# Kernel optimization log

Hardware: AMD Instinct MI355X
Metric: run time of the kernel (lower is better)

The kernel has to match this reference:

```python
import jax, jax.numpy as jnp
import numpy as np

D_MODEL = 512
N_HEADS = 8
D_HEAD = D_MODEL // N_HEADS
N_BINS = 32


def setup_inputs() -> dict:
    key = jax.random.key(0)
    ks = jax.random.split(key, 12)
    B, N = 8, 1024
    x = jax.random.normal(ks[0], (B, N, D_MODEL), dtype=jnp.float32)
    positions = jax.random.randint(ks[1], (B, N), 0, 5000, dtype=jnp.int32)
    mask = jnp.ones((B, N), dtype=jnp.float32)
    s = 0.02
    qw = jax.random.normal(ks[2], (D_MODEL, D_MODEL), jnp.float32) * s
    qb = jnp.zeros((D_MODEL,), jnp.float32)
    kw = jax.random.normal(ks[3], (D_MODEL, D_MODEL), jnp.float32) * s
    kb = jnp.zeros((D_MODEL,), jnp.float32)
    vw = jax.random.normal(ks[4], (D_MODEL, D_MODEL), jnp.float32) * s
    vb = jnp.zeros((D_MODEL,), jnp.float32)
    ow = jax.random.normal(ks[5], (D_MODEL, D_MODEL), jnp.float32) * s
    ob = jnp.zeros((D_MODEL,), jnp.float32)
    dist_emb = jax.random.normal(ks[6], (N_BINS, N_HEADS), jnp.float32) * s
    order_bias = jnp.zeros((N_HEADS,), jnp.float32)
    bin_edges = jnp.logspace(0.0, 3.0, N_BINS - 1, dtype=jnp.float32)
    return {"x": x, "positions": positions, "mask": mask,
            "qw": qw, "qb": qb, "kw": kw, "kb": kb, "vw": vw, "vb": vb,
            "ow": ow, "ob": ob, "dist_emb": dist_emb, "order_bias": order_bias,
            "bin_edges": bin_edges}


def reference(x, positions, mask, qw, qb, kw, kb, vw, vb, ow, ob, dist_emb, order_bias, bin_edges):
    B, N, _ = x.shape
    scale = jnp.sqrt(jnp.float32(D_HEAD))
    # projections (torch Linear: y = x @ W^T + b), split heads -> (B,H,N,Dh)
    q = (x @ qw.T + qb).reshape(B, N, N_HEADS, D_HEAD).transpose(0, 2, 1, 3)
    k = (x @ kw.T + kb).reshape(B, N, N_HEADS, D_HEAD).transpose(0, 2, 1, 3)
    v = (x @ vw.T + vb).reshape(B, N, N_HEADS, D_HEAD).transpose(0, 2, 1, 3)
    scores = jnp.einsum('bhqd,bhkd->bhqk', q, k) / scale  # (B,H,N,N)
    pos = positions.astype(jnp.float32)
    pos_i = pos[:, :, None]   # (B,N,1)
    pos_j = pos[:, None, :]   # (B,1,N)
    dist = jnp.abs(pos_j - pos_i)  # (B,N,N)
    # torch.bucketize(right=False) == searchsorted side='left'
    bins = jnp.clip(jnp.searchsorted(bin_edges, dist, side='left'), 0, N_BINS - 1)
    dist_bias = dist_emb[bins]  # (B,N,N,H)
    scores = scores + dist_bias.transpose(0, 3, 1, 2)
    order_sign = (pos_j > pos_i).astype(scores.dtype) - 0.5  # (B,N,N)
    scores = scores + order_sign[:, None, :, :] * order_bias[None, :, None, None]
    mask_2d = mask[:, None, None, :] * mask[:, None, :, None]  # (B,1,N,N)
    scores = jnp.where(mask_2d == 0, jnp.float32(-1e9), scores)
    attn = jax.nn.softmax(scores, axis=-1)
    attn = jnp.nan_to_num(attn, nan=0.0)
    out = jnp.einsum('bhqk,bhkd->bhqd', attn, v)
    out = out.transpose(0, 2, 1, 3).reshape(B, N, D_MODEL)
    out = out * mask[..., None]
    return out @ ow.T + ob
```

## Files before the change

### kernel.cpp

```cpp
#include <hip/hip_runtime.h>
#include <hip/hip_bf16.h>

#define SEQ   1024
#define NH    8
#define DH    64

typedef __attribute__((ext_vector_type(8))) _Float16 half8;
typedef __attribute__((ext_vector_type(4))) _Float16 half4;
typedef __attribute__((ext_vector_type(4))) float    f32x4;

#if __has_builtin(__builtin_amdgcn_exp2f)
#define EXP2F __builtin_amdgcn_exp2f
#else
#define EXP2F exp2f
#endif

__device__ inline unsigned pk2(float a, float b) {
  return __builtin_bit_cast(unsigned, __builtin_amdgcn_cvt_pkrtz(a, b));
}
__device__ inline void swap32(unsigned &a, unsigned &b) {
  asm("v_permlane32_swap_b32 %0, %1" : "+v"(a), "+v"(b));
}
__device__ inline void swap16(unsigned &a, unsigned &b) {
  asm("v_permlane16_swap_b32 %0, %1" : "+v"(a), "+v"(b));
}
__device__ inline half8 mk8(unsigned a, unsigned b, unsigned c, unsigned d) {
  union { unsigned u[4]; half8 h; } x;
  x.u[0] = a; x.u[1] = b; x.u[2] = c; x.u[3] = d;
  return x.h;
}
__device__ __forceinline__ void gload16(const _Float16* g, _Float16* l) {
  __builtin_amdgcn_global_load_lds((const __attribute__((address_space(1))) void*)g,
                                   (__attribute__((address_space(3))) void*)l, 16, 0, 0);
}

__global__ void prep_all(const float* __restrict__ x,
                         const float* __restrict__ qw, const float* __restrict__ kw,
                         const float* __restrict__ vw, const float* __restrict__ ow,
                         const float* __restrict__ qb, const float* __restrict__ kb,
                         const float* __restrict__ vb, const float* __restrict__ edges,
                         _Float16* __restrict__ xh, _Float16* __restrict__ wqkvh,
                         _Float16* __restrict__ owh, float* __restrict__ qkvbias,
                         unsigned char* __restrict__ lutd) {
  const int blk = blockIdx.x, tid = threadIdx.x;
  if (blk < 4096) {
    int g = blk * 256 + tid;
    float4 v = reinterpret_cast<const float4*>(x)[g];
    half4 u;
    u[0] = (_Float16)v.x; u[1] = (_Float16)v.y; u[2] = (_Float16)v.z; u[3] = (_Float16)v.w;
    reinterpret_cast<half4*>(xh)[g] = u;
  } else if (blk < 5122) {
    int g = (blk - 4096) * 256 + tid;
    if (g < 196608) {
      const float* src = (g < 65536) ? qw : (g < 131072) ? kw : vw;
      int lg = g & 65535;
      float4 v = reinterpret_cast<const float4*>(src)[lg];
      half4 u;
      u[0] = (_Float16)v.x; u[1] = (_Float16)v.y; u[2] = (_Float16)v.z; u[3] = (_Float16)v.w;
      reinterpret_cast<half4*>(wqkvh)[g] = u;
    } else if (g < 262144) {
      int lg = g - 196608;
      float4 v = reinterpret_cast<const float4*>(ow)[lg];
      half4 u;
      u[0] = (_Float16)v.x; u[1] = (_Float16)v.y; u[2] = (_Float16)v.z; u[3] = (_Float16)v.w;
      reinterpret_cast<half4*>(owh)[lg] = u;
    } else if (g < 262528) {
      int lg = g - 262144;
      const float* src = (lg < 128) ? qb : (lg < 256) ? kb : vb;
      int ll = lg & 127;
      reinterpret_cast<float4*>(qkvbias)[lg] = reinterpret_cast<const float4*>(src)[ll];
    }
  } else {
    int d = (blk - 5122) * 256 + tid;
    float fd = (float)d;
    int bin = 0;
#pragma unroll
    for (int t = 0; t < 31; ++t) bin += (edges[t] < fd) ? 1 : 0;
    lutd[d] = (unsigned char)bin;
  }
}

__global__ __launch_bounds__(256) void prep_ebins(const int* __restrict__ positions,
                                                  const float* __restrict__ mask,
                                                  const unsigned char* __restrict__ lutd,
                                                  unsigned char* __restrict__ ebins) {
  __shared__ unsigned char lutl[5120];
  __shared__ int posl[SEQ];
  __shared__ unsigned char mk[SEQ];
  const int b = blockIdx.x >> 8, j0 = (blockIdx.x & 255) * 4;
  const int tid = threadIdx.x;
  for (int i = tid; i < 1280; i += 256)
    reinterpret_cast<unsigned*>(lutl)[i] = reinterpret_cast<const unsigned*>(lutd)[i];
  for (int i = tid; i < SEQ; i += 256) {
    posl[i] = positions[b * SEQ + i];
    mk[i] = (mask[b * SEQ + i] == 0.f) ? 32 : 0;
  }
  __syncthreads();
  const int c0 = tid * 4;
#pragma unroll
  for (int jj = 0; jj < 4; ++jj) {
    const int j = j0 + jj;
    const int pr = posl[j];
    unsigned out = 0;
#pragma unroll
    for (int r = 0; r < 4; ++r) {
      int c = c0 + r;
      int pc = posl[c];
      int d = pc - pr; d = d < 0 ? -d : d;
      if (d > 5119) d = 5119;
      unsigned e = lutl[d] | (unsigned)mk[c] | ((pc > pr) ? 64u : 0u);
      out |= e << (8 * r);
    }
    reinterpret_cast<unsigned*>(&ebins[(size_t)(b * SEQ + j) * SEQ])[tid] = out;
  }
}

__global__ __launch_bounds__(256) void qkv_gemm3(const _Float16* __restrict__ xh,
                                                 const _Float16* __restrict__ wh,
                                                 const float* __restrict__ bias,
                                                 _Float16* __restrict__ qkv) {
  __shared__ __attribute__((aligned(16))) _Float16 As[128 * 64];
  __shared__ __attribute__((aligned(16))) _Float16 Bs[128 * 64];
  const int m0 = blockIdx.x * 128, n0 = blockIdx.y * 128;
  const int tid = threadIdx.x, w = tid >> 6, lane = tid & 63;
  const int lr = lane & 15, lg = lane >> 4;
  const int wr = (w >> 1) * 64, wc = (w & 1) * 64;
  f32x4 acc[4][4] = {};
  const int srow8 = lane >> 3;
  const int scol = ((lane & 7) ^ srow8) * 8;
  for (int k0 = 0; k0 < 512; k0 += 64) {
#pragma unroll
    for (int j = 0; j < 4; ++j) {
      const int row = (w * 4 + j) * 8 + srow8;
      gload16(&xh[(size_t)(m0 + row) * 512 + k0 + scol], &As[(w * 4 + j) * 512]);
      gload16(&wh[(size_t)(n0 + row) * 512 + k0 + scol], &Bs[(w * 4 + j) * 512]);
    }
    __syncthreads();
#pragma unroll
    for (int kk = 0; kk < 2; ++kk) {
      half8 af[4], bf[4];
#pragma unroll
      for (int mt = 0; mt < 4; ++mt) {
        const int row = wr + mt * 16 + lr;
        af[mt] = *reinterpret_cast<const half8*>(
            (const char*)As + row * 128 + (((kk * 4 + lg) ^ (row & 7)) * 16));
      }
#pragma unroll
      for (int nt = 0; nt < 4; ++nt) {
        const int row = wc + nt * 16 + lr;
        bf[nt] = *reinterpret_cast<const half8*>(
            (const char*)Bs + row * 128 + (((kk * 4 + lg) ^ (row & 7)) * 16));
      }
#pragma unroll
      for (int mt = 0; mt < 4; ++mt)
#pragma unroll
        for (int nt = 0; nt < 4; ++nt)
          acc[mt][nt] = __builtin_amdgcn_mfma_f32_16x16x32_f16(af[mt], bf[nt], acc[mt][nt], 0, 0, 0);
    }
    __syncthreads();
  }
  const int p = n0 >> 9;
  const float scl = (p == 0) ? 0.125f : (p == 1) ? 1.44269504f : 1.0f;
  if (p < 2) {
#pragma unroll
    for (int nt = 0; nt < 4; ++nt) {
      int n = n0 + wc + nt * 16 + lr;
      float bv = bias[n];
      int c = n & 511, h = c >> 6, d = c & 63;
#pragma unroll
      for (int mt = 0; mt < 4; ++mt)
#pragma unroll
        for (int r = 0; r < 4; ++r) {
          int m = m0 + wr + mt * 16 + lg * 4 + r;
          int bb = m >> 10, nn = m & 1023;
          qkv[p * 4194304 + ((bb * NH + h) * SEQ + nn) * DH + d] = (_Float16)((acc[mt][nt][r] + bv) * scl);
        }
    }
  } else {
#pragma unroll
    for (int nt = 0; nt < 4; ++nt) {
      int n = n0 + wc + nt * 16 + lr;
      float bv = bias[n];
      int c = n & 511, h = c >> 6, d = c & 63;
#pragma unroll
      for (int mt = 0; mt < 4; ++mt) {
        int m = m0 + wr + mt * 16 + lg * 4;
        int bb = m >> 10, nn = m & 1023;
        half4 st;
#pragma unroll
        for (int r = 0; r < 4; ++r) st[r] = (_Float16)(acc[mt][nt][r] + bv);
        *reinterpret_cast<half4*>(&qkv[8388608 + ((bb * NH + h) * DH + d) * SEQ + nn]) = st;
      }
    }
  }
}

#define ASTAGE(bufi, kv0_) do {                                                              \
    _Pragma("unroll") for (int j = 0; j < 2; ++j) {                                          \
      const int row_ = (w * 2 + j) * 8 + (lane >> 3);                                        \
      const int c_ = ((lane & 7) ^ (row_ & 7)) * 8;                                          \
      gload16(Kg + (size_t)((kv0_) + row_) * 64 + c_, &Ks[bufi][(w * 2 + j) * 512]);         \
      gload16(Vtg + (size_t)row_ * 1024 + (kv0_) + c_, &Vt[bufi][(w * 2 + j) * 512]);        \
    }                                                                                        \
  } while (0)

#define EBL(dst, kt_) do {                                                                   \
    _Pragma("unroll") for (int ct = 0; ct < 4; ++ct)                                         \
      dst[ct] = *reinterpret_cast<const unsigned*>(                                          \
          &ebins[(size_t)(b * SEQ + q_base + lr) * SEQ + (kt_) * 64 + ct * 16 + lg * 4]);    \
  } while (0)

#define ACOMP(bufi, ebw) do {                                                                \
    f32x4 s[4];                                                                              \
    _Pragma("unroll") for (int ct = 0; ct < 4; ++ct) {                                       \
      const unsigned eb_ = ebw[ct];                                                          \
      _Pragma("unroll") for (int r = 0; r < 4; ++r) {                                        \
        const unsigned i6_ = (eb_ >> (8 * r)) & 63u;                      \
        float bias_ = elut2[i6_];                                                            \
        if (obh_nz) bias_ += ((eb_ >> (8 * r)) & 64u) ? obh : -obh;                          \
        s[ct][r] = bias_;                                                                    \
      }                                                                                      \
    }                                                                                        \
    __builtin_amdgcn_s_setprio(1);                                                           \
    _Pragma("unroll") for (int ct = 0; ct < 4; ++ct) {                                       \
      const int krow_ = ct * 16 + lr;                                                        \
      half8 kf0 = *reinterpret_cast<const half8*>(                                           \
          (const char*)&Ks[bufi][0] + krow_ * 128 + ((lg ^ (krow_ & 7)) * 16));              \
      half8 kf1 = *reinterpret_cast<const half8*>(                                           \
          (const char*)&Ks[bufi][0] + krow_ * 128 + (((4 + lg) ^ (krow_ & 7)) * 16));        \
      s[ct] = __builtin_amdgcn_mfma_f32_16x16x32_f16(kf0, qf[0], s[ct], 0, 0, 0);            \
      s[ct] = __builtin_amdgcn_mfma_f32_16x16x32_f16(kf1, qf[1], s[ct], 0, 0, 0);            \
    }                                                                                        \
    __builtin_amdgcn_s_setprio(0);                                                           \
                 \
    unsigned W[4][2];                                                                        \
    _Pragma("unroll") for (int ct = 0; ct < 4; ++ct) {                                       \
      float p0 = EXP2F(s[ct][0]), p1 = EXP2F(s[ct][1]);                                      \
      float p2 = EXP2F(s[ct][2]), p3 = EXP2F(s[ct][3]);                                      \
      l_run += (p0 + p1) + (p2 + p3);                                                        \
      W[ct][0] = pk2(p0, p1);                                                                \
      W[ct][1] = pk2(p2, p3);                                                                \
    }                                                                                        \
    swap32(W[0][0], W[1][0]); swap32(W[0][1], W[1][1]);                                      \
    swap32(W[2][0], W[3][0]); swap32(W[2][1], W[3][1]);                                      \
    swap16(W[0][0], W[1][0]); swap16(W[0][1], W[1][1]);                                      \
    swap16(W[2][0], W[3][0]); swap16(W[2][1], W[3][1]);                                      \
    __builtin_amdgcn_s_setprio(1);                                                           \
    _Pragma("unroll") for (int ks = 0; ks < 2; ++ks) {                                       \
      half8 pa = mk8(W[ks * 2][0], W[ks * 2][1], W[ks * 2 + 1][0], W[ks * 2 + 1][1]);        \
      _Pragma("unroll") for (int dt = 0; dt < 4; ++dt) {                                     \
        const int vrow_ = dt * 16 + lr;                                                      \
        half8 vf = *reinterpret_cast<const half8*>(                                          \
            (const char*)&Vt[bufi][0] + vrow_ * 128 + (((ks * 4 + lg) ^ (vrow_ & 7)) * 16)); \
        o[dt] = __builtin_amdgcn_mfma_f32_16x16x32_f16(vf, pa, o[dt], 0, 0, 0);              \
      }                                                                                      \
    }                                                                                        \
    __builtin_amdgcn_s_setprio(0);                                                           \
  } while (0)

__global__ __launch_bounds__(256, 4) void attn8(const _Float16* __restrict__ qkv,
                                                const float* __restrict__ mask,
                                                const unsigned char* __restrict__ ebins,
                                                const float* __restrict__ demb,
                                                const float* __restrict__ obias,
                                                _Float16* __restrict__ aout) {
  __shared__ __attribute__((aligned(16))) _Float16 Ks[2][64 * 64];
  __shared__ __attribute__((aligned(16))) _Float16 Vt[2][64 * 64];
  __shared__ float elut2[64];

  const int blk = blockIdx.x;
  const int lin = (blk & 7) * 128 + (blk >> 3);
  const int qt = lin & 15, h = (lin >> 4) & 7, b = lin >> 7;
  const int tid = threadIdx.x, w = tid >> 6, lane = tid & 63;
  const int lr = lane & 15, lg = lane >> 4;

  if (tid < 64) elut2[tid] = (tid < 32) ? demb[tid * NH + h] * 1.44269504f : -1.442695e9f;
  const float obh = 0.5f * obias[h] * 1.44269504f;
  const bool obh_nz = (obh != 0.f);

  const _Float16* Qg  = qkv + (size_t)(b * NH + h) * 65536;
  const _Float16* Kg  = qkv + 4194304 + (size_t)(b * NH + h) * 65536;
  const _Float16* Vtg = qkv + 8388608 + (size_t)(b * NH + h) * 65536;

  const int q_base = qt * 64 + w * 16;
  half8 qf[2];
#pragma unroll
  for (int ks = 0; ks < 2; ++ks)
    qf[ks] = *reinterpret_cast<const half8*>(&Qg[(q_base + lr) * DH + ks * 32 + lg * 8]);
  const float mq = mask[b * SEQ + q_base + lr];

  float l_run = 0.f;
  f32x4 o[4] = {};

  unsigned ebwA[4], ebwB[4];
  EBL(ebwA, 0);
  ASTAGE(0, 0);
  __syncthreads();

#pragma unroll 1
  for (int i = 0; i < 8; ++i) {
    const int kt = 2 * i;
    EBL(ebwB, kt + 1);
    ASTAGE(1, (kt + 1) * 64);
    ACOMP(0, ebwA);
    __syncthreads();
    if (kt + 2 < 16) {
      EBL(ebwA, kt + 2);
      ASTAGE(0, (kt + 2) * 64);
    }
    ACOMP(1, ebwB);
    __syncthreads();
  }

  float s_ = l_run;
  s_ += __shfl_xor(s_, 16);
  s_ += __shfl_xor(s_, 32);
  const float linv = mq / fmaxf(s_, 1e-35f);
#pragma unroll
  for (int dt = 0; dt < 4; ++dt) {
    half4 st;
#pragma unroll
    for (int r = 0; r < 4; ++r) st[r] = (_Float16)(o[dt][r] * linv);
    *reinterpret_cast<half4*>(
        &aout[(size_t)(b * SEQ + q_base + lr) * 512 + h * DH + dt * 16 + lg * 4]) = st;
  }
}

__global__ __launch_bounds__(256) void out_gemm3(const _Float16* __restrict__ ah,
                                                 const _Float16* __restrict__ wh,
                                                 const float* __restrict__ ob,
                                                 float* __restrict__ out) {
  __shared__ __attribute__((aligned(16))) _Float16 As[128 * 64];
  __shared__ __attribute__((aligned(16))) _Float16 Bs[64 * 64];
  const int m0 = blockIdx.x * 128, n0 = blockIdx.y * 64;
  const int tid = threadIdx.x, w = tid >> 6, lane = tid & 63;
  const int lr = lane & 15, lg = lane >> 4;
  const int wr = (w >> 1) * 64, wc = (w & 1) * 32;
  f32x4 acc[4][2] = {};
  const int srow8 = lane >> 3;
  const int scol = ((lane & 7) ^ srow8) * 8;
  for (int k0 = 0; k0 < 512; k0 += 64) {
#pragma unroll
    for (int j = 0; j < 4; ++j) {
      const int row = (w * 4 + j) * 8 + srow8;
      gload16(&ah[(size_t)(m0 + row) * 512 + k0 + scol], &As[(w * 4 + j) * 512]);
    }
#pragma unroll
    for (int j = 0; j < 2; ++j) {
      const int row = (w * 2 + j) * 8 + srow8;
      gload16(&wh[(size_t)(n0 + row) * 512 + k0 + scol], &Bs[(w * 2 + j) * 512]);
    }
    __syncthreads();
#pragma unroll
    for (int kk = 0; kk < 2; ++kk) {
      half8 af[4], bf[2];
#pragma unroll
      for (int mt = 0; mt < 4; ++mt) {
        const int row = wr + mt * 16 + lr;
        af[mt] = *reinterpret_cast<const half8*>(
            (const char*)As + row * 128 + (((kk * 4 + lg) ^ (row & 7)) * 16));
      }
#pragma unroll
      for (int nt = 0; nt < 2; ++nt) {
        const int row = wc + nt * 16 + lr;
        bf[nt] = *reinterpret_cast<const half8*>(
            (const char*)Bs + row * 128 + (((kk * 4 + lg) ^ (row & 7)) * 16));
      }
#pragma unroll
      for (int mt = 0; mt < 4; ++mt)
#pragma unroll
        for (int nt = 0; nt < 2; ++nt)
          acc[mt][nt] = __builtin_amdgcn_mfma_f32_16x16x32_f16(af[mt], bf[nt], acc[mt][nt], 0, 0, 0);
    }
    __syncthreads();
  }
#pragma unroll
  for (int nt = 0; nt < 2; ++nt) {
    int n = n0 + wc + nt * 16 + lr;
    float bv = ob[n];
#pragma unroll
    for (int mt = 0; mt < 4; ++mt)
#pragma unroll
      for (int r = 0; r < 4; ++r) {
        int m = m0 + wr + mt * 16 + lg * 4 + r;
        out[m * 512 + n] = acc[mt][nt][r] + bv;
      }
  }
}

extern "C" void kernel_launch(void* const* d_in, const int* in_sizes, int n_in,
                              void* d_out, int out_size, void* d_ws, size_t ws_size,
                              hipStream_t stream) {
  const float* x         = (const float*)d_in[0];
  const int*   positions = (const int*)d_in[1];
  const float* mask      = (const float*)d_in[2];
  const float* qw        = (const float*)d_in[3];
  const float* qb        = (const float*)d_in[4];
  const float* kw        = (const float*)d_in[5];
  const float* kb        = (const float*)d_in[6];
  const float* vw        = (const float*)d_in[7];
  const float* vb        = (const float*)d_in[8];
  const float* ow        = (const float*)d_in[9];
  const float* ob        = (const float*)d_in[10];
  const float* demb      = (const float*)d_in[11];
  const float* obias     = (const float*)d_in[12];
  const float* edges     = (const float*)d_in[13];

  char* ws = (char*)d_ws;
  _Float16* xh        = (_Float16*)(ws);
  unsigned char* ebins = (unsigned char*)(ws);
  _Float16* qkv       = (_Float16*)(ws + 8388608);
  _Float16* aouth     = (_Float16*)(ws + 33554432);
  _Float16* wqkvh     = (_Float16*)(ws + 41943040);
  _Float16* owh       = (_Float16*)(ws + 43515904);
  float*    qkvbias   = (float*)(ws + 44040192);
  unsigned char* lutd = (unsigned char*)(ws + 44046336);
  float*    outp      = (float*)d_out;

  prep_all<<<5142, 256, 0, stream>>>(x, qw, kw, vw, ow, qb, kb, vb, edges,
                                     xh, wqkvh, owh, qkvbias, lutd);
  qkv_gemm3<<<dim3(64, 12), 256, 0, stream>>>(xh, wqkvh, qkvbias, qkv);
  prep_ebins<<<2048, 256, 0, stream>>>(positions, mask, lutd, ebins);
  attn8<<<1024, 256, 0, stream>>>(qkv, mask, ebins, demb, obias, aouth);
  out_gemm3<<<dim3(64, 8), 256, 0, stream>>>(aouth, owh, ob, outp);
}
```

Measured before the change: 102.5 us.

## Fuse x fp16 conversion into QKV GEMM, shrink GEMM tiles, relax attention barriers

The QKV GEMM now reads fp32 x directly, converts it to fp16 in registers and writes it into swizzled LDS. This drops the separate x conversion pass and its round trip through the workspace. Both GEMMs move to 64-row M tiles, doubling the grid to fill more CUs. The attention loop issues the async K/V stage before the ebins loads and replaces __syncthreads with a barrier that waits only until vmcnt(4). That partial wait risks correctness if the outstanding-load count does not match what each stage needs. Kernel launch order is also changed so prep_ebins runs before the QKV GEMM.

```diff
diff --git a/kernel.cpp b/kernel.cpp
--- a/kernel.cpp
+++ b/kernel.cpp
@@ -34,23 +34,22 @@
                                    (__attribute__((address_space(3))) void*)l, 16, 0, 0);
 }
 
-__global__ void prep_all(const float* __restrict__ x,
-                         const float* __restrict__ qw, const float* __restrict__ kw,
+#define BARRIER4 do {                                        \
+    __builtin_amdgcn_sched_barrier(0);                       \
+    asm volatile("s_waitcnt vmcnt(4)" ::: "memory");         \
+    __builtin_amdgcn_s_barrier();                            \
+    __builtin_amdgcn_sched_barrier(0);                       \
+  } while (0)
+
+__global__ void prep_all(const float* __restrict__ qw, const float* __restrict__ kw,
                          const float* __restrict__ vw, const float* __restrict__ ow,
                          const float* __restrict__ qb, const float* __restrict__ kb,
                          const float* __restrict__ vb, const float* __restrict__ edges,
-                         _Float16* __restrict__ xh, _Float16* __restrict__ wqkvh,
-                         _Float16* __restrict__ owh, float* __restrict__ qkvbias,
-                         unsigned char* __restrict__ lutd) {
+                         _Float16* __restrict__ wqkvh, _Float16* __restrict__ owh,
+                         float* __restrict__ qkvbias, unsigned char* __restrict__ lutd) {
   const int blk = blockIdx.x, tid = threadIdx.x;
-  if (blk < 4096) {
+  if (blk < 1026) {
     int g = blk * 256 + tid;
-    float4 v = reinterpret_cast<const float4*>(x)[g];
-    half4 u;
-    u[0] = (_Float16)v.x; u[1] = (_Float16)v.y; u[2] = (_Float16)v.z; u[3] = (_Float16)v.w;
-    reinterpret_cast<half4*>(xh)[g] = u;
-  } else if (blk < 5122) {
-    int g = (blk - 4096) * 256 + tid;
     if (g < 196608) {
       const float* src = (g < 65536) ? qw : (g < 131072) ? kw : vw;
       int lg = g & 65535;
@@ -71,7 +70,7 @@
       reinterpret_cast<float4*>(qkvbias)[lg] = reinterpret_cast<const float4*>(src)[ll];
     }
   } else {
-    int d = (blk - 5122) * 256 + tid;
+    int d = (blk - 1026) * 256 + tid;
     float fd = (float)d;
     int bin = 0;
 #pragma unroll
@@ -115,32 +114,45 @@
   }
 }
 
-__global__ __launch_bounds__(256) void qkv_gemm3(const _Float16* __restrict__ xh,
+__global__ __launch_bounds__(256) void qkv_gemm4(const float* __restrict__ x,
                                                  const _Float16* __restrict__ wh,
                                                  const float* __restrict__ bias,
                                                  _Float16* __restrict__ qkv) {
-  __shared__ __attribute__((aligned(16))) _Float16 As[128 * 64];
+  __shared__ __attribute__((aligned(16))) _Float16 As[64 * 64];
   __shared__ __attribute__((aligned(16))) _Float16 Bs[128 * 64];
-  const int m0 = blockIdx.x * 128, n0 = blockIdx.y * 128;
+  const int m0 = blockIdx.x * 64, n0 = blockIdx.y * 128;
   const int tid = threadIdx.x, w = tid >> 6, lane = tid & 63;
   const int lr = lane & 15, lg = lane >> 4;
-  const int wr = (w >> 1) * 64, wc = (w & 1) * 64;
-  f32x4 acc[4][4] = {};
+  const int wr = (w >> 1) * 32, wc = (w & 1) * 64;
+  f32x4 acc[2][4] = {};
+  const int arow = tid >> 2, aq = (tid & 3) * 16;
+  const int ach0 = ((tid & 3) * 2) ^ (arow & 7);
   const int srow8 = lane >> 3;
   const int scol = ((lane & 7) ^ srow8) * 8;
   for (int k0 = 0; k0 < 512; k0 += 64) {
+    const float* xr = &x[(size_t)(m0 + arow) * 512 + k0 + aq];
+    float4 f0 = *reinterpret_cast<const float4*>(xr);
+    float4 f1 = *reinterpret_cast<const float4*>(xr + 4);
+    float4 f2 = *reinterpret_cast<const float4*>(xr + 8);
+    float4 f3 = *reinterpret_cast<const float4*>(xr + 12);
+    uint4 st0, st1;
+    st0.x = pk2(f0.x, f0.y); st0.y = pk2(f0.z, f0.w);
+    st0.z = pk2(f1.x, f1.y); st0.w = pk2(f1.z, f1.w);
+    st1.x = pk2(f2.x, f2.y); st1.y = pk2(f2.z, f2.w);
+    st1.z = pk2(f3.x, f3.y); st1.w = pk2(f3.z, f3.w);
+    *reinterpret_cast<uint4*>((char*)As + arow * 128 + ach0 * 16) = st0;
+    *reinterpret_cast<uint4*>((char*)As + arow * 128 + (ach0 ^ 1) * 16) = st1;
 #pragma unroll
     for (int j = 0; j < 4; ++j) {
       const int row = (w * 4 + j) * 8 + srow8;
-      gload16(&xh[(size_t)(m0 + row) * 512 + k0 + scol], &As[(w * 4 + j) * 512]);
       gload16(&wh[(size_t)(n0 + row) * 512 + k0 + scol], &Bs[(w * 4 + j) * 512]);
     }
     __syncthreads();
 #pragma unroll
     for (int kk = 0; kk < 2; ++kk) {
-      half8 af[4], bf[4];
-#pragma unroll
-      for (int mt = 0; mt < 4; ++mt) {
+      half8 af[2], bf[4];
+#pragma unroll
+      for (int mt = 0; mt < 2; ++mt) {
         const int row = wr + mt * 16 + lr;
         af[mt] = *reinterpret_cast<const half8*>(
             (const char*)As + row * 128 + (((kk * 4 + lg) ^ (row & 7)) * 16));
@@ -152,7 +164,7 @@
             (const char*)Bs + row * 128 + (((kk * 4 + lg) ^ (row & 7)) * 16));
       }
 #pragma unroll
-      for (int mt = 0; mt < 4; ++mt)
+      for (int mt = 0; mt < 2; ++mt)
 #pragma unroll
         for (int nt = 0; nt < 4; ++nt)
           acc[mt][nt] = __builtin_amdgcn_mfma_f32_16x16x32_f16(af[mt], bf[nt], acc[mt][nt], 0, 0, 0);
@@ -168,7 +180,7 @@
       float bv = bias[n];
       int c = n & 511, h = c >> 6, d = c & 63;
 #pragma unroll
-      for (int mt = 0; mt < 4; ++mt)
+      for (int mt = 0; mt < 2; ++mt)
 #pragma unroll
         for (int r = 0; r < 4; ++r) {
           int m = m0 + wr + mt * 16 + lg * 4 + r;
@@ -183,7 +195,7 @@
       float bv = bias[n];
       int c = n & 511, h = c >> 6, d = c & 63;
 #pragma unroll
-      for (int mt = 0; mt < 4; ++mt) {
+      for (int mt = 0; mt < 2; ++mt) {
         int m = m0 + wr + mt * 16 + lg * 4;
         int bb = m >> 10, nn = m & 1023;
         half4 st;
@@ -258,7 +270,7 @@
     __builtin_amdgcn_s_setprio(0);                                                           \
   } while (0)
 
-__global__ __launch_bounds__(256, 4) void attn8(const _Float16* __restrict__ qkv,
+__global__ __launch_bounds__(256, 4) void attn9(const _Float16* __restrict__ qkv,
                                                 const float* __restrict__ mask,
                                                 const unsigned char* __restrict__ ebins,
                                                 const float* __restrict__ demb,
@@ -293,23 +305,23 @@
   f32x4 o[4] = {};
 
   unsigned ebwA[4], ebwB[4];
+  ASTAGE(0, 0);
   EBL(ebwA, 0);
-  ASTAGE(0, 0);
   __syncthreads();
 
 #pragma unroll 1
   for (int i = 0; i < 8; ++i) {
     const int kt = 2 * i;
+    ASTAGE(1, (kt + 1) * 64);
     EBL(ebwB, kt + 1);
-    ASTAGE(1, (kt + 1) * 64);
     ACOMP(0, ebwA);
-    __syncthreads();
+    BARRIER4;
     if (kt + 2 < 16) {
+      ASTAGE(0, (kt + 2) * 64);
       EBL(ebwA, kt + 2);
-      ASTAGE(0, (kt + 2) * 64);
     }
     ACOMP(1, ebwB);
-    __syncthreads();
+    BARRIER4;
   }
 
   float s_ = l_run;
@@ -326,36 +338,32 @@
   }
 }
 
-__global__ __launch_bounds__(256) void out_gemm3(const _Float16* __restrict__ ah,
+__global__ __launch_bounds__(256) void out_gemm4(const _Float16* __restrict__ ah,
                                                  const _Float16* __restrict__ wh,
                                                  const float* __restrict__ ob,
                                                  float* __restrict__ out) {
-  __shared__ __attribute__((aligned(16))) _Float16 As[128 * 64];
+  __shared__ __attribute__((aligned(16))) _Float16 As[64 * 64];
   __shared__ __attribute__((aligned(16))) _Float16 Bs[64 * 64];
-  const int m0 = blockIdx.x * 128, n0 = blockIdx.y * 64;
+  const int m0 = blockIdx.x * 64, n0 = blockIdx.y * 64;
   const int tid = threadIdx.x, w = tid >> 6, lane = tid & 63;
   const int lr = lane & 15, lg = lane >> 4;
-  const int wr = (w >> 1) * 64, wc = (w & 1) * 32;
-  f32x4 acc[4][2] = {};
+  const int wr = (w >> 1) * 32, wc = (w & 1) * 32;
+  f32x4 acc[2][2] = {};
   const int srow8 = lane >> 3;
   const int scol = ((lane & 7) ^ srow8) * 8;
   for (int k0 = 0; k0 < 512; k0 += 64) {
 #pragma unroll
-    for (int j = 0; j < 4; ++j) {
-      const int row = (w * 4 + j) * 8 + srow8;
-      gload16(&ah[(size_t)(m0 + row) * 512 + k0 + scol], &As[(w * 4 + j) * 512]);
-    }
-#pragma unroll
     for (int j = 0; j < 2; ++j) {
       const int row = (w * 2 + j) * 8 + srow8;
+      gload16(&ah[(size_t)(m0 + row) * 512 + k0 + scol], &As[(w * 2 + j) * 512]);
       gload16(&wh[(size_t)(n0 + row) * 512 + k0 + scol], &Bs[(w * 2 + j) * 512]);
     }
     __syncthreads();
 #pragma unroll
     for (int kk = 0; kk < 2; ++kk) {
-      half8 af[4], bf[2];
-#pragma unroll
-      for (int mt = 0; mt < 4; ++mt) {
+      half8 af[2], bf[2];
+#pragma unroll
+      for (int mt = 0; mt < 2; ++mt) {
         const int row = wr + mt * 16 + lr;
         af[mt] = *reinterpret_cast<const half8*>(
             (const char*)As + row * 128 + (((kk * 4 + lg) ^ (row & 7)) * 16));
@@ -367,7 +375,7 @@
             (const char*)Bs + row * 128 + (((kk * 4 + lg) ^ (row & 7)) * 16));
       }
 #pragma unroll
-      for (int mt = 0; mt < 4; ++mt)
+      for (int mt = 0; mt < 2; ++mt)
 #pragma unroll
         for (int nt = 0; nt < 2; ++nt)
           acc[mt][nt] = __builtin_amdgcn_mfma_f32_16x16x32_f16(af[mt], bf[nt], acc[mt][nt], 0, 0, 0);
@@ -379,7 +387,7 @@
     int n = n0 + wc + nt * 16 + lr;
     float bv = ob[n];
 #pragma unroll
-    for (int mt = 0; mt < 4; ++mt)
+    for (int mt = 0; mt < 2; ++mt)
 #pragma unroll
       for (int r = 0; r < 4; ++r) {
         int m = m0 + wr + mt * 16 + lg * 4 + r;
@@ -407,7 +415,6 @@
   const float* edges     = (const float*)d_in[13];
 
   char* ws = (char*)d_ws;
-  _Float16* xh        = (_Float16*)(ws);
   unsigned char* ebins = (unsigned char*)(ws);
   _Float16* qkv       = (_Float16*)(ws + 8388608);
   _Float16* aouth     = (_Float16*)(ws + 33554432);
@@ -417,10 +424,10 @@
   unsigned char* lutd = (unsigned char*)(ws + 44046336);
   float*    outp      = (float*)d_out;
 
-  prep_all<<<5142, 256, 0, stream>>>(x, qw, kw, vw, ow, qb, kb, vb, edges,
-                                     xh, wqkvh, owh, qkvbias, lutd);
-  qkv_gemm3<<<dim3(64, 12), 256, 0, stream>>>(xh, wqkvh, qkvbias, qkv);
+  prep_all<<<1046, 256, 0, stream>>>(qw, kw, vw, ow, qb, kb, vb, edges,
+                                     wqkvh, owh, qkvbias, lutd);
   prep_ebins<<<2048, 256, 0, stream>>>(positions, mask, lutd, ebins);
-  attn8<<<1024, 256, 0, stream>>>(qkv, mask, ebins, demb, obias, aouth);
-  out_gemm3<<<dim3(64, 8), 256, 0, stream>>>(aouth, owh, ob, outp);
-}
+  qkv_gemm4<<<dim3(128, 12), 256, 0, stream>>>(x, wqkvh, qkvbias, qkv);
+  attn9<<<1024, 256, 0, stream>>>(qkv, mask, ebins, demb, obias, aouth);
+  out_gemm4<<<dim3(128, 8), 256, 0, stream>>>(aouth, owh, ob, outp);
+}
```

Result: slower. 109.5 us (+6.9%).
